# Kernel optimization log

Measured on AMD Instinct MI355X. Metric: run time of the kernel, lower is better.

The kernel has to match this reference:

```python
import jax, jax.numpy as jnp
import numpy as np

N, E, G = 8192, 65536, 16          # atoms, edges, graphs in batch
NUM_ELEM, C, NB = 10, 64, 8        # elements, hidden channels, bessel basis
LMAX, NLAYERS = 3, 2
LM = (LMAX + 1) ** 2               # 16 spherical-harmonic components
R_MAX, P_CUT = 5.0, 5
EPS = 1e-9


def spherical_harmonics(u):
    # u: [E,3] unit vectors -> real spherical harmonics l<=3, [E,16]
    x, y, z = u[:, 0], u[:, 1], u[:, 2]
    x2, y2, z2 = x * x, y * y, z * z
    sh = [
        jnp.full_like(x, 0.28209479177387814),
        0.4886025119029199 * y, 0.4886025119029199 * z, 0.4886025119029199 * x,
        1.0925484305920792 * x * y, 1.0925484305920792 * y * z,
        0.31539156525252005 * (3.0 * z2 - 1.0),
        1.0925484305920792 * x * z, 0.5462742152960396 * (x2 - y2),
        0.5900435899266435 * y * (3.0 * x2 - y2), 2.890611442640554 * x * y * z,
        0.4570457994644658 * y * (5.0 * z2 - 1.0),
        0.3731763325901154 * z * (5.0 * z2 - 3.0),
        0.4570457994644658 * x * (5.0 * z2 - 1.0),
        1.445305721320277 * z * (x2 - y2),
        0.5900435899266435 * x * (x2 - 3.0 * y2),
    ]
    return jnp.stack(sh, axis=-1)


def radial_embedding(r):
    # Bessel radial basis with polynomial envelope cutoff -> [E, NB]
    u = r / R_MAX
    p = float(P_CUT)
    cut = (1.0 - 0.5 * (p + 1.0) * (p + 2.0) * u ** P_CUT
           + p * (p + 2.0) * u ** (P_CUT + 1)
           - 0.5 * p * (p + 1.0) * u ** (P_CUT + 2))
    cut = jnp.where(u < 1.0, cut, 0.0)
    n = jnp.arange(1, NB + 1, dtype=r.dtype)
    bessel = jnp.sqrt(2.0 / R_MAX) * jnp.sin(n[None, :] * jnp.pi * u[:, None]) \
             / jnp.maximum(r, EPS)[:, None]
    return bessel * cut[:, None]


def setup_inputs() -> dict:
    key = jax.random.key(0)
    ks = jax.random.split(key, 10)
    positions = jax.random.uniform(ks[0], (N, 3), jnp.float32) * 10.0
    elems = jax.random.randint(ks[1], (N,), 0, NUM_ELEM)
    node_attrs = jax.nn.one_hot(elems, NUM_ELEM, dtype=jnp.float32)
    edge_index = jax.random.randint(ks[2], (2, E), 0, N).astype(jnp.int32)
    shifts = jnp.zeros((E, 3), jnp.float32)
    batch = jnp.sort(jax.random.randint(ks[3], (N,), 0, G)).astype(jnp.int32)
    W_embed = jax.random.normal(ks[4], (NUM_ELEM, C), jnp.float32) / np.sqrt(NUM_ELEM)
    atomic_energies_w = jnp.arange(-1.0, -(NUM_ELEM + 1.0), -1.0, dtype=jnp.float32)
    W_rad = jax.random.normal(ks[5], (NLAYERS, NB, C), jnp.float32) / np.sqrt(NB)
    W_prod = jax.random.normal(ks[6], (NLAYERS, NUM_ELEM, (LMAX + 1) * C, C),
                               jnp.float32) / np.sqrt((LMAX + 1) * C)
    w_read = jax.random.normal(ks[7], (C,), jnp.float32) / np.sqrt(C)
    return {"positions": positions, "node_attrs": node_attrs, "shifts": shifts,
            "W_embed": W_embed, "atomic_energies_w": atomic_energies_w,
            "W_rad": W_rad, "W_prod": W_prod, "w_read": w_read,
            "edge_index": edge_index, "batch": batch}


def _energy(positions, node_attrs, shifts, W_embed, atomic_energies_w,
            W_rad, W_prod, w_read, edge_index, batch):
    snd, rcv = edge_index[0], edge_index[1]
    vec = positions[rcv] - positions[snd] + shifts            # [E,3]
    length = jnp.sqrt(jnp.sum(vec * vec, axis=-1) + EPS)      # [E]
    Y = spherical_harmonics(vec / length[:, None])            # [E,LM]
    R = radial_embedding(length)                              # [E,NB]

    e0 = jax.ops.segment_sum(node_attrs @ atomic_energies_w, batch, num_segments=G)
    h = node_attrs @ W_embed                                  # [N,C]

    for layer in range(NLAYERS):
        w = R @ W_rad[layer]                                  # [E,C] radial weights
        msg = (w * h[snd])[:, None, :] * Y[:, :, None]        # [E,LM,C] tensor product
        A = jax.ops.segment_sum(msg, rcv, num_segments=N)     # [N,LM,C] atomic basis
        A2 = A * A
        # invariant (rotation-invariant) contraction: sum over m within each l
        B = jnp.concatenate(
            [A2[:, l * l:(l + 1) * (l + 1), :].sum(axis=1) for l in range(LMAX + 1)],
            axis=-1)                                          # [N,(LMAX+1)*C]
        # element-dependent product-basis mixing
        h = jnp.einsum('nf,efc,ne->nc', B, W_prod[layer], node_attrs)

    node_e = h @ w_read                                       # [N]
    inter_e = jax.ops.segment_sum(node_e, batch, num_segments=G)
    return e0 + inter_e                                       # [G]


def reference(positions, node_attrs, shifts, W_embed, atomic_energies_w,
              W_rad, W_prod, w_read, edge_index, batch):
    energy = _energy(positions, node_attrs, shifts, W_embed, atomic_energies_w,
                     W_rad, W_prod, w_read, edge_index, batch)
    forces = -jax.grad(
        lambda p: _energy(p, node_attrs, shifts, W_embed, atomic_energies_w,
                          W_rad, W_prod, w_read, edge_index, batch).sum()
    )(positions)
    return energy, forces
```

## Files before the change

kernel.cpp:

```cpp
#include <hip/hip_runtime.h>
#include <math.h>

#define NN 8192
#define NE 65536
#define NG 16
#define NEL 10
#define CC 64
#define NLM 16
#define MAXST 32
#define PI_F 3.14159265358979f

__device__ __forceinline__ int lm_l(int lm) {
    return (lm == 0) ? 0 : (lm < 4) ? 1 : (lm < 9) ? 2 : 3;
}

__device__ __forceinline__ void stage_pack(
    const float* __restrict__ PK, const int* __restrict__ SSND,
    int beg, int cnt, int c, float* sPK, int* sS)
{
    int tot = cnt * 24;
    for (int i = c; i < tot; i += 64) sPK[i] = PK[(size_t)beg*24 + i];
    if (c < cnt) sS[c] = SSND[beg + c];
    __builtin_amdgcn_wave_barrier();
}

__global__ __launch_bounds__(256) void k_front(
    const float* __restrict__ pos, const float* __restrict__ shifts,
    const int* __restrict__ snd, const int* __restrict__ rcv,
    float* __restrict__ Y, float* __restrict__ R,
    float* __restrict__ U, float* __restrict__ L, int* __restrict__ cnt,
    const float* __restrict__ attrs, const float* __restrict__ Wemb,
    const float* __restrict__ aew, const int* __restrict__ batch,
    float* __restrict__ h0, int* __restrict__ elem, int* __restrict__ ecnt,
    float* __restrict__ out,
    const float* __restrict__ Wprod1, const float* __restrict__ wread,
    float* __restrict__ vb1)
{
    __shared__ int hcnt[NEL];
    int bx = blockIdx.x;
    if (bx < 256) {
        int e = bx * 256 + threadIdx.x;
        int s = snd[e], r = rcv[e];
        float vx = pos[r*3+0] - pos[s*3+0] + shifts[e*3+0];
        float vy = pos[r*3+1] - pos[s*3+1] + shifts[e*3+1];
        float vz = pos[r*3+2] - pos[s*3+2] + shifts[e*3+2];
        float len = sqrtf(vx*vx + vy*vy + vz*vz + 1e-9f);
        L[e] = len;
        if (len >= 5.0f) return;
        atomicAdd(&cnt[r], 1);
        float x = vx/len, y = vy/len, z = vz/len;
        U[e*3+0] = x; U[e*3+1] = y; U[e*3+2] = z;
        float x2 = x*x, y2 = y*y, z2 = z*z;
        float4* Yv = (float4*)(Y + (size_t)e*16);
        Yv[0] = make_float4(0.28209479177387814f,
                            0.4886025119029199f*y,
                            0.4886025119029199f*z,
                            0.4886025119029199f*x);
        Yv[1] = make_float4(1.0925484305920792f*x*y,
                            1.0925484305920792f*y*z,
                            0.31539156525252005f*(3.f*z2 - 1.f),
                            1.0925484305920792f*x*z);
        Yv[2] = make_float4(0.5462742152960396f*(x2 - y2),
                            0.5900435899266435f*y*(3.f*x2 - y2),
                            2.890611442640554f*x*y*z,
                            0.4570457994644658f*y*(5.f*z2 - 1.f));
        Yv[3] = make_float4(0.3731763325901154f*z*(5.f*z2 - 3.f),
                            0.4570457994644658f*x*(5.f*z2 - 1.f),
                            1.445305721320277f*z*(x2 - y2),
                            0.5900435899266435f*x*(x2 - 3.f*y2));
        float ur = len * 0.2f;
        float u2 = ur*ur, u4 = u2*u2, u5 = u4*ur, u6 = u5*ur, u7 = u6*ur;
        float cut = 1.f - 21.f*u5 + 35.f*u6 - 15.f*u7;
        const float s2f = 0.632455532033676f;
        float th = (PI_F/5.f) * len;
        float s1, c1; sincosf(th, &s1, &c1);
        float sn_ = s1, cs = c1;
        float coef = s2f * cut / len;
        float rv[8];
#pragma unroll
        for (int nb = 0; nb < 8; nb++) {
            rv[nb] = coef * sn_;
            float ns = sn_*c1 + cs*s1;
            float nc = cs*c1 - sn_*s1;
            sn_ = ns; cs = nc;
        }
        float4* Rv = (float4*)(R + (size_t)e*8);
        Rv[0] = make_float4(rv[0], rv[1], rv[2], rv[3]);
        Rv[1] = make_float4(rv[4], rv[5], rv[6], rv[7]);
    } else if (bx < 768) {
        int t = threadIdx.x, c = t & 63, w = t >> 6;
        if (t < NEL) hcnt[t] = 0;
        __syncthreads();
        float esum = 0.f; int curb = -1;
        for (int g = 0; g < 4; g++) {
            int n = (bx - 256)*16 + w*4 + g;
            float hv = 0.f;
            for (int el = 0; el < NEL; el++) hv += attrs[n*NEL+el] * Wemb[el*CC+c];
            h0[(size_t)n*CC+c] = hv;
            int el = 0; float e0 = 0.f;
            for (int k = 0; k < NEL; k++) {
                float a = attrs[n*NEL+k];
                e0 += a * aew[k];
                if (a > 0.5f) el = k;
            }
            if (c == 0) {
                elem[n] = el;
                atomicAdd(&hcnt[el], 1);
            }
            int b = batch[n];
            if (b != curb) {
                if (curb >= 0 && c == 0) atomicAdd(&out[curb], esum);
                curb = b; esum = 0.f;
            }
            esum += e0;
        }
        if (curb >= 0 && c == 0) atomicAdd(&out[curb], esum);
        __syncthreads();
        if (t < NEL) { int v = hcnt[t]; if (v) atomicAdd(&ecnt[t], v); }
    } else {
        int el = bx - 768, f = threadIdx.x;
        float s = 0.f;
        for (int c = 0; c < CC; c++) s += wread[c] * Wprod1[(size_t)el*256*CC + f*CC + c];
        vb1[el*256+f] = s;
    }
}

__global__ __launch_bounds__(1024) void k_scan(
    const int* __restrict__ cnt, int* __restrict__ offs,
    const int* __restrict__ ecnt, int* __restrict__ eoff)
{
    __shared__ int wsum[16];
    int t = threadIdx.x, lane = t & 63, w = t >> 6;
    int loc[8];
    int run = 0;
#pragma unroll
    for (int i = 0; i < 8; i++) { int v = cnt[t*8+i]; loc[i] = run; run += v; }
    int v = run;
#pragma unroll
    for (int o = 1; o < 64; o <<= 1) {
        int u = __shfl_up(v, o, 64);
        if (lane >= o) v += u;
    }
    if (lane == 63) wsum[w] = v;
    __syncthreads();
    if (t < 16) {
        int x = wsum[t];
#pragma unroll
        for (int o = 1; o < 16; o <<= 1) {
            int u = __shfl_up(x, o, 64);
            if (t >= o) x += u;
        }
        wsum[t] = x;
    }
    __syncthreads();
    int wpre = (w == 0) ? 0 : wsum[w-1];
    int pre = wpre + v - run;
#pragma unroll
    for (int i = 0; i < 8; i++) offs[t*8+i] = pre + loc[i];
    if (t == 1023) offs[NN] = pre + run;
    if (t == 0) {
        int r = 0;
        for (int el = 0; el < NEL; el++) { eoff[el] = r; r += ecnt[el]; }
        eoff[NEL] = r;
    }
}

__global__ void k_scatpack(
    const int* __restrict__ snd, const int* __restrict__ rcv,
    const float* __restrict__ Y, const float* __restrict__ R,
    const float* __restrict__ U, const float* __restrict__ L,
    const int* __restrict__ offs, int* __restrict__ cur,
    float* __restrict__ PK, int* __restrict__ SSND, int* __restrict__ SRCV,
    float* __restrict__ UL,
    const int* __restrict__ elem, const int* __restrict__ eoff,
    int* __restrict__ ecur, int* __restrict__ nbe)
{
    int e = blockIdx.x * blockDim.x + threadIdx.x;
    if (e < NN) {
        int el = elem[e];
        int p = eoff[el] + atomicAdd(&ecur[el], 1);
        nbe[p] = e;
    }
    if (e >= NE) return;
    if (L[e] >= 5.0f) return;
    int r = rcv[e];
    int p = offs[r] + atomicAdd(&cur[r], 1);
    const float4* Yp = (const float4*)(Y + (size_t)e*16);
    float4* d = (float4*)(PK + (size_t)p*24);
    d[0] = Yp[0]; d[1] = Yp[1]; d[2] = Yp[2]; d[3] = Yp[3];
    const float4* Rp = (const float4*)(R + (size_t)e*8);
    d[4] = Rp[0]; d[5] = Rp[1];
    SSND[p] = snd[e];
    SRCV[p] = rcv[e];
    ((float4*)UL)[p] = make_float4(U[e*3+0], U[e*3+1], U[e*3+2], L[e]);
}

__global__ __launch_bounds__(256) void k_fwd0(
    const float* __restrict__ PK, const int* __restrict__ SSND,
    const float* __restrict__ Wrad0, const float* __restrict__ Wprod0,
    const float* __restrict__ h0, const float* __restrict__ attrs,
    const int* __restrict__ elem, const int* __restrict__ offs,
    const int* __restrict__ nbe, float* __restrict__ h1,
    float* __restrict__ A0)
{
    __shared__ __align__(16) float sB[4][1024];
    __shared__ __align__(16) float sPK[4][MAXST*24];
    __shared__ int sS[4][MAXST];
    int t = threadIdx.x, c = t & 63, w = t >> 6;
    float wr[8];
#pragma unroll
    for (int nb = 0; nb < 8; nb++) wr[nb] = Wrad0[nb*CC+c];
    int nid[4], nel[4]; float na[4];
#pragma unroll
    for (int g = 0; g < 4; g++) {
        int n = nbe[blockIdx.x*16 + w*4 + g];
        nid[g] = n;
        int el = elem[n]; nel[g] = el; na[g] = attrs[n*NEL+el];
        float acc[NLM];
#pragma unroll
        for (int lm = 0; lm < NLM; lm++) acc[lm] = 0.f;
        int beg = offs[n], end = offs[n+1];
        for (int base = beg; base < end; base += MAXST) {
            int m = min(MAXST, end - base);
            stage_pack(PK, SSND, base, m, c, sPK[w], sS[w]);
            for (int cb = 0; cb < m; cb += 4) {
                float hb[4];
#pragma unroll
                for (int k = 0; k < 4; k++)
                    hb[k] = (cb+k < m) ? h0[(size_t)sS[w][cb+k]*CC + c] : 0.f;
#pragma unroll
                for (int jj = 0; jj < 4; jj++) {
                    if (cb+jj >= m) break;
                    const float* rec = &sPK[w][(cb+jj)*24];
                    float wv = 0.f;
#pragma unroll
                    for (int nb = 0; nb < 8; nb++) wv += rec[16+nb]*wr[nb];
                    float tt = wv * hb[jj];
#pragma unroll
                    for (int lm = 0; lm < NLM; lm++) acc[lm] += rec[lm]*tt;
                }
            }
            __builtin_amdgcn_wave_barrier();
        }
#pragma unroll
        for (int lm = 0; lm < NLM; lm++) A0[(size_t)n*1024 + lm*64 + c] = acc[lm];
        float b0 = acc[0]*acc[0];
        float b1 = acc[1]*acc[1] + acc[2]*acc[2] + acc[3]*acc[3];
        float b2 = acc[4]*acc[4] + acc[5]*acc[5] + acc[6]*acc[6] + acc[7]*acc[7] + acc[8]*acc[8];
        float b3 = 0.f;
#pragma unroll
        for (int lm = 9; lm < 16; lm++) b3 += acc[lm]*acc[lm];
        sB[w][g*256 + 0*64 + c] = b0;
        sB[w][g*256 + 1*64 + c] = b1;
        sB[w][g*256 + 2*64 + c] = b2;
        sB[w][g*256 + 3*64 + c] = b3;
    }
    __builtin_amdgcn_wave_barrier();
    float hv[4] = {0.f, 0.f, 0.f, 0.f};
    int done = 0;
    while (done != 0xF) {
        int g0 = __ffs(~done & 0xF) - 1;
        int el = (g0==0) ? nel[0] : (g0==1) ? nel[1] : (g0==2) ? nel[2] : nel[3];
        int msk = 0;
#pragma unroll
        for (int g = 0; g < 4; g++) if (nel[g] == el) msk |= 1 << g;
        const float* Wn = Wprod0 + (size_t)el*256*CC;
        float tmp[4] = {0.f, 0.f, 0.f, 0.f};
        for (int f4 = 0; f4 < 64; f4++) {
            float wv0 = Wn[(f4*4+0)*CC + c];
            float wv1 = Wn[(f4*4+1)*CC + c];
            float wv2 = Wn[(f4*4+2)*CC + c];
            float wv3 = Wn[(f4*4+3)*CC + c];
#pragma unroll
            for (int g = 0; g < 4; g++) {
                float4 b = *((const float4*)&sB[w][g*256 + f4*4]);
                tmp[g] += b.x*wv0 + b.y*wv1 + b.z*wv2 + b.w*wv3;
            }
        }
#pragma unroll
        for (int g = 0; g < 4; g++) if ((msk >> g) & 1) hv[g] = tmp[g];
        done |= msk;
    }
#pragma unroll
    for (int g = 0; g < 4; g++) h1[(size_t)nid[g]*CC + c] = na[g]*hv[g];
}

__global__ __launch_bounds__(256) void k_gseed(
    const float* __restrict__ gh1, const float* __restrict__ Wprod0,
    const float* __restrict__ attrs, const int* __restrict__ elem,
    const int* __restrict__ nbe, float* __restrict__ GB)
{
    __shared__ __align__(16) float sgh[4][4][64];
    int t = threadIdx.x, c = t & 63, w = t >> 6;
    int nid[4], nel[4]; float na[4];
#pragma unroll
    for (int g = 0; g < 4; g++) {
        int n = nbe[blockIdx.x*16 + w*4 + g];
        nid[g] = n;
        int el = elem[n]; nel[g] = el; na[g] = attrs[n*NEL+el];
        sgh[w][g][c] = gh1[(size_t)n*CC + c];
    }
    __builtin_amdgcn_wave_barrier();
    float outv[4][4];
    int done = 0;
    while (done != 0xF) {
        int g0 = __ffs(~done & 0xF) - 1;
        int el = (g0==0) ? nel[0] : (g0==1) ? nel[1] : (g0==2) ? nel[2] : nel[3];
        int msk = 0;
#pragma unroll
        for (int g = 0; g < 4; g++) if (nel[g] == el) msk |= 1 << g;
        const float* W0 = Wprod0 + (size_t)el*256*CC;
#pragma unroll
        for (int l = 0; l < 4; l++) {
            const float4* row = (const float4*)(W0 + (size_t)(l*64 + c)*CC);
            float t4[4] = {0.f, 0.f, 0.f, 0.f};
#pragma unroll 4
            for (int k4 = 0; k4 < 16; k4++) {
                float4 wv = row[k4];
#pragma unroll
                for (int g = 0; g < 4; g++) {
                    float4 gg = *((const float4*)&sgh[w][g][k4*4]);
                    t4[g] += wv.x*gg.x + wv.y*gg.y + wv.z*gg.z + wv.w*gg.w;
                }
            }
#pragma unroll
            for (int g = 0; g < 4; g++) if ((msk >> g) & 1) outv[l][g] = t4[g];
        }
        done |= msk;
    }
#pragma unroll
    for (int g = 0; g < 4; g++)
#pragma unroll
        for (int l = 0; l < 4; l++)
            GB[(size_t)nid[g]*256 + l*64 + c] = na[g]*outv[l][g];
}

__global__ __launch_bounds__(256) void k_fbwd(
    const float* __restrict__ PK, const int* __restrict__ SSND,
    const float* __restrict__ Wrad, const float* __restrict__ hprev,
    const float* __restrict__ vb1, const float* __restrict__ GB,
    const float* __restrict__ A0,
    const float* __restrict__ attrs, const int* __restrict__ elem,
    const int* __restrict__ batch, const int* __restrict__ offs,
    float* __restrict__ gYp, float* __restrict__ gRp, float* __restrict__ gh,
    float* __restrict__ out, int layer1)
{
    __shared__ __align__(16) float wrls[8*68];
    __shared__ __align__(16) float sPK[4][MAXST*24];
    __shared__ int sS[4][MAXST];
    __shared__ __align__(16) float Mls[4][16*68];
    __shared__ __align__(16) float Tls[4][4*68];
    __shared__ __align__(16) float Gls[4][4*68];
    int t = threadIdx.x, c = t & 63, w = t >> 6;
    float wr[8];
#pragma unroll
    for (int nb = 0; nb < 8; nb++) wr[nb] = Wrad[nb*CC+c];
    if (w == 0) {
#pragma unroll
        for (int nb = 0; nb < 8; nb++) wrls[nb*68+c] = wr[nb];
    }
    __syncthreads();
    float esum = 0.f; int curb = -1;
    for (int g = 0; g < 4; g++) {
        int n = blockIdx.x*16 + w*4 + g;
        int el = elem[n];
        float a = attrs[n*NEL+el];
        float g4[4];
        if (layer1) {
#pragma unroll
            for (int l = 0; l < 4; l++) g4[l] = a * vb1[el*256 + l*64 + c];
        } else {
#pragma unroll
            for (int l = 0; l < 4; l++) g4[l] = GB[(size_t)n*256 + l*64 + c];
        }
        int beg = offs[n], end = offs[n+1];
        int cnt = end - beg;
        float acc[NLM];
        bool cached = false;
        if (layer1) {
#pragma unroll
            for (int lm = 0; lm < NLM; lm++) acc[lm] = 0.f;
            for (int base = beg; base < end; base += MAXST) {
                int m = min(MAXST, end - base);
                stage_pack(PK, SSND, base, m, c, sPK[w], sS[w]);
                for (int cb = 0; cb < m; cb += 4) {
                    float hb[4];
#pragma unroll
                    for (int k = 0; k < 4; k++)
                        hb[k] = (cb+k < m) ? hprev[(size_t)sS[w][cb+k]*CC + c] : 0.f;
#pragma unroll
                    for (int jj = 0; jj < 4; jj++) {
                        if (cb+jj >= m) break;
                        const float* rec = &sPK[w][(cb+jj)*24];
                        float wv = 0.f;
#pragma unroll
                        for (int nb = 0; nb < 8; nb++) wv += rec[16+nb]*wr[nb];
                        float tt = wv * hb[jj];
#pragma unroll
                        for (int lm = 0; lm < NLM; lm++) acc[lm] += rec[lm]*tt;
                    }
                }
                __builtin_amdgcn_wave_barrier();
            }
            cached = (cnt <= MAXST);
            float b0 = acc[0]*acc[0];
            float b1 = acc[1]*acc[1] + acc[2]*acc[2] + acc[3]*acc[3];
            float b2 = acc[4]*acc[4] + acc[5]*acc[5] + acc[6]*acc[6] + acc[7]*acc[7] + acc[8]*acc[8];
            float b3 = 0.f;
#pragma unroll
            for (int lm = 9; lm < 16; lm++) b3 += acc[lm]*acc[lm];
            float ep = b0*vb1[el*256+c] + b1*vb1[el*256+64+c]
                     + b2*vb1[el*256+128+c] + b3*vb1[el*256+192+c];
#pragma unroll
            for (int o = 32; o > 0; o >>= 1) ep += __shfl_xor(ep, o, 64);
            int b = batch[n];
            if (b != curb) {
                if (curb >= 0 && c == 0) atomicAdd(&out[curb], esum);
                curb = b; esum = 0.f;
            }
            esum += a * ep;
        } else {
#pragma unroll
            for (int lm = 0; lm < NLM; lm++) acc[lm] = A0[(size_t)n*1024 + lm*64 + c];
        }
        float M[NLM];
#pragma unroll
        for (int lm = 0; lm < NLM; lm++) {
            M[lm] = 2.f * acc[lm] * g4[lm_l(lm)];
            Mls[w][lm*68+c] = M[lm];
        }
        __builtin_amdgcn_wave_barrier();
        for (int base = beg; base < end; base += MAXST) {
            int m = min(MAXST, end - base);
            if (!cached) stage_pack(PK, SSND, base, m, c, sPK[w], sS[w]);
            for (int cb = 0; cb < m; cb += 4) {
                int ncq = min(4, m - cb);
                float hb[4];
#pragma unroll
                for (int k = 0; k < 4; k++)
                    hb[k] = (cb+k < m) ? hprev[(size_t)sS[w][cb+k]*CC + c] : 0.f;
#pragma unroll
                for (int jj = 0; jj < 4; jj++) {
                    if (jj >= ncq) break;
                    const float* rec = &sPK[w][(cb+jj)*24];
                    float wv = 0.f;
#pragma unroll
                    for (int nb = 0; nb < 8; nb++) wv += rec[16+nb]*wr[nb];
                    float hvv = hb[jj];
                    float my = 0.f;
#pragma unroll
                    for (int lm = 0; lm < NLM; lm++) my += M[lm]*rec[lm];
                    Tls[w][jj*68+c] = wv * hvv;
                    Gls[w][jj*68+c] = hvv * my;
                    if (layer1) atomicAdd(&gh[(size_t)sS[w][cb+jj]*CC + c], wv * my);
                }
                __builtin_amdgcn_wave_barrier();
                {
                    int jj = c >> 4, lm = c & 15;
                    if (jj < ncq) {
                        const float4* mrow = (const float4*)&Mls[w][lm*68];
                        const float4* trow = (const float4*)&Tls[w][jj*68];
                        float s_ = 0.f;
#pragma unroll
                        for (int k4 = 0; k4 < 16; k4++) {
                            float4 mm = mrow[k4]; float4 tv = trow[k4];
                            s_ += mm.x*tv.x + mm.y*tv.y + mm.z*tv.z + mm.w*tv.w;
                        }
                        size_t p = (size_t)(base + cb + jj);
                        if (layer1) gYp[p*16+lm] = s_;
                        else        gYp[p*16+lm] += s_;
                    }
                }
                if (c < 32) {
                    int jj = c >> 3, nb = c & 7;
                    if (jj < ncq) {
                        const float4* wrow = (const float4*)&wrls[nb*68];
                        const float4* grow = (const float4*)&Gls[w][jj*68];
                        float s_ = 0.f;
#pragma unroll
                        for (int k4 = 0; k4 < 16; k4++) {
                            float4 wv4 = wrow[k4]; float4 gv = grow[k4];
                            s_ += wv4.x*gv.x + wv4.y*gv.y + wv4.z*gv.z + wv4.w*gv.w;
                        }
                        size_t p = (size_t)(base + cb + jj);
                        if (layer1) gRp[p*8+nb] = s_;
                        else        gRp[p*8+nb] += s_;
                    }
                }
                __builtin_amdgcn_wave_barrier();
            }
        }
    }
    if (curb >= 0 && c == 0) atomicAdd(&out[curb], esum);
}

__global__ void k_geo_bwd(const float* __restrict__ gYp, const float* __restrict__ gRp,
                          const float* __restrict__ UL, const int* __restrict__ SSND,
                          const int* __restrict__ SRCV, const int* __restrict__ offs,
                          float* __restrict__ F)
{
    int p = blockIdx.x * blockDim.x + threadIdx.x;
    if (p >= offs[NN]) return;
    float4 ul = ((const float4*)UL)[p];
    float x = ul.x, y = ul.y, z = ul.z, len = ul.w;
    float g[16];
    {
        const float4* gv = (const float4*)(gYp + (size_t)p*16);
        float4 a0 = gv[0], a1 = gv[1], a2 = gv[2], a3 = gv[3];
        g[0]=a0.x; g[1]=a0.y; g[2]=a0.z; g[3]=a0.w;
        g[4]=a1.x; g[5]=a1.y; g[6]=a1.z; g[7]=a1.w;
        g[8]=a2.x; g[9]=a2.y; g[10]=a2.z; g[11]=a2.w;
        g[12]=a3.x; g[13]=a3.y; g[14]=a3.z; g[15]=a3.w;
    }
    float gr[8];
    {
        const float4* rv = (const float4*)(gRp + (size_t)p*8);
        float4 r0 = rv[0], r1 = rv[1];
        gr[0]=r0.x; gr[1]=r0.y; gr[2]=r0.z; gr[3]=r0.w;
        gr[4]=r1.x; gr[5]=r1.y; gr[6]=r1.z; gr[7]=r1.w;
    }
    float x2 = x*x, y2 = y*y, z2 = z*z;
    float gx = 0.f, gy = 0.f, gz = 0.f;
    gx += 0.4886025119029199f*g[3];
    gy += 0.4886025119029199f*g[1];
    gz += 0.4886025119029199f*g[2];
    gx += 1.0925484305920792f*y*g[4];  gy += 1.0925484305920792f*x*g[4];
    gy += 1.0925484305920792f*z*g[5];  gz += 1.0925484305920792f*y*g[5];
    gz += 1.8923493915151203f*z*g[6];
    gx += 1.0925484305920792f*z*g[7];  gz += 1.0925484305920792f*x*g[7];
    gx += 1.0925484305920792f*x*g[8];  gy -= 1.0925484305920792f*y*g[8];
    gx += 3.540261539559861f*x*y*g[9];
    gy += 0.5900435899266435f*(3.f*x2 - 3.f*y2)*g[9];
    gx += 2.890611442640554f*y*z*g[10]; gy += 2.890611442640554f*x*z*g[10]; gz += 2.890611442640554f*x*y*g[10];
    gy += 0.4570457994644658f*(5.f*z2 - 1.f)*g[11]; gz += 4.570457994644658f*y*z*g[11];
    gz += 0.3731763325901154f*(15.f*z2 - 3.f)*g[12];
    gx += 0.4570457994644658f*(5.f*z2 - 1.f)*g[13]; gz += 4.570457994644658f*x*z*g[13];
    gx += 2.890611442640554f*x*z*g[14]; gy -= 2.890611442640554f*y*z*g[14];
    gz += 1.445305721320277f*(x2 - y2)*g[14];
    gx += 0.5900435899266435f*(3.f*x2 - 3.f*y2)*g[15];
    gy -= 3.540261539559861f*x*y*g[15];
    float ur = len * 0.2f;
    float gL = 0.f;
    {
        float u2 = ur*ur, u4 = u2*u2, u5 = u4*ur, u6 = u5*ur, u7 = u6*ur;
        float poly  = 1.f - 21.f*u5 + 35.f*u6 - 15.f*u7;
        float dpoly = (-105.f*u4 + 210.f*u5 - 105.f*u6)*0.2f;
        const float s2f = 0.632455532033676f;
        const float k1 = PI_F/5.f;
        float th = k1*len;
        float s1, c1; sincosf(th, &s1, &c1);
        float sn_ = s1, cs = c1;
        float inv_r = 1.f/len;
        bool tiny = (len < 2e-3f);
#pragma unroll
        for (int nb = 0; nb < 8; nb++) {
            float kn = k1*(float)(nb+1);
            float bes = s2f*sn_*inv_r;
            float dbes;
            if (tiny) dbes = -s2f*kn*kn*kn*len*(1.f/3.f);
            else      dbes = s2f*(kn*cs - sn_*inv_r)*inv_r;
            gL += gr[nb]*(dbes*poly + bes*dpoly);
            float ns = sn_*c1 + cs*s1;
            float nc = cs*c1 - sn_*s1;
            sn_ = ns; cs = nc;
        }
    }
    float dot = gx*x + gy*y + gz*z;
    float gvx = (gx - dot*x)/len + gL*x;
    float gvy = (gy - dot*y)/len + gL*y;
    float gvz = (gz - dot*z)/len + gL*z;
    int sn = SSND[p], rn = SRCV[p];
    atomicAdd(&F[rn*3+0], -gvx);
    atomicAdd(&F[rn*3+1], -gvy);
    atomicAdd(&F[rn*3+2], -gvz);
    atomicAdd(&F[sn*3+0],  gvx);
    atomicAdd(&F[sn*3+1],  gvy);
    atomicAdd(&F[sn*3+2],  gvz);
}

extern "C" void kernel_launch(void* const* d_in, const int* in_sizes, int n_in,
                              void* d_out, int out_size, void* d_ws, size_t ws_size,
                              hipStream_t stream)
{
    const float* positions  = (const float*)d_in[0];
    const float* node_attrs = (const float*)d_in[1];
    const float* shifts     = (const float*)d_in[2];
    const float* W_embed    = (const float*)d_in[3];
    const float* aew        = (const float*)d_in[4];
    const float* W_rad      = (const float*)d_in[5];
    const float* W_prod     = (const float*)d_in[6];
    const float* w_read     = (const float*)d_in[7];
    const int*   edge_index = (const int*)d_in[8];
    const int*   batch      = (const int*)d_in[9];
    float* out = (float*)d_out;

    const int* snd = edge_index;
    const int* rcv = edge_index + NE;

    char* ws = (char*)d_ws;
    size_t off = 0;
    auto allocf = [&](size_t nelems) -> float* {
        float* p = (float*)(ws + off); off += nelems * sizeof(float); return p;
    };
    float* Y    = allocf((size_t)NE*16);
    float* R    = allocf((size_t)NE*8);
    float* U    = allocf((size_t)NE*3);
    float* L    = allocf((size_t)NE);
    float* PK   = allocf((size_t)NE*24);
    float* UL   = allocf((size_t)NE*4);
    float* H0   = allocf((size_t)NN*CC);
    float* H1   = allocf((size_t)NN*CC);
    float* A0   = allocf((size_t)NN*1024);
    float* GYP  = allocf((size_t)NE*16);
    float* GRP  = allocf((size_t)NE*8);
    float* GB   = allocf((size_t)NN*256);
    float* VB1  = allocf((size_t)NEL*256);
    size_t zero_off = off;
    float* GH1  = allocf((size_t)NN*CC);
    int* CNT   = (int*)(ws + off); off += (size_t)NN*4;
    int* CUR   = (int*)(ws + off); off += (size_t)NN*4;
    int* ECNT  = (int*)(ws + off); off += 16*4;
    int* ECUR  = (int*)(ws + off); off += 16*4;
    size_t zero_bytes = off - zero_off;
    int* ELEM  = (int*)(ws + off); off += (size_t)NN*4;
    int* OFFS  = (int*)(ws + off); off += (size_t)(NN+1)*4;
    int* SSND  = (int*)(ws + off); off += (size_t)NE*4;
    int* SRCV  = (int*)(ws + off); off += (size_t)NE*4;
    int* ELOFF = (int*)(ws + off); off += 16*4;
    int* NBE   = (int*)(ws + off); off += (size_t)NN*4;

    hipMemsetAsync(out, 0, (size_t)out_size * sizeof(float), stream);
    hipMemsetAsync(ws + zero_off, 0, zero_bytes, stream);

    const float* Wrad0  = W_rad;
    const float* Wrad1  = W_rad + 8*CC;
    const float* Wprod0 = W_prod;
    const float* Wprod1 = W_prod + (size_t)NEL*256*CC;

    k_front<<<256 + 512 + NEL, 256, 0, stream>>>(
        positions, shifts, snd, rcv, Y, R, U, L, CNT,
        node_attrs, W_embed, aew, batch, H0, ELEM, ECNT, out,
        Wprod1, w_read, VB1);
    k_scan<<<1, 1024, 0, stream>>>(CNT, OFFS, ECNT, ELOFF);
    k_scatpack<<<NE/256, 256, 0, stream>>>(snd, rcv, Y, R, U, L, OFFS, CUR,
                                           PK, SSND, SRCV, UL, ELEM, ELOFF, ECUR, NBE);

    k_fwd0<<<NN/16, 256, 0, stream>>>(PK, SSND, Wrad0, Wprod0, H0, node_attrs, ELEM,
                                      OFFS, NBE, H1, A0);
    k_fbwd<<<NN/16, 256, 0, stream>>>(PK, SSND, Wrad1, H1, VB1, GB, A0, node_attrs, ELEM,
                                      batch, OFFS, GYP, GRP, GH1, out, 1);
    k_gseed<<<NN/16, 256, 0, stream>>>(GH1, Wprod0, node_attrs, ELEM, NBE, GB);
    k_fbwd<<<NN/16, 256, 0, stream>>>(PK, SSND, Wrad0, H0, VB1, GB, A0, node_attrs, ELEM,
                                      batch, OFFS, GYP, GRP, GH1, out, 0);

    k_geo_bwd<<<NE/256, 256, 0, stream>>>(GYP, GRP, UL, SSND, SRCV, OFFS, out + NG);
    (void)in_sizes; (void)n_in; (void)ws_size;
}
```

Before: 288.1 us.

## Fuse gradient seed, layer-0 backward and geometric force backward into one kernel

Splits the shared backward kernel into a layer-1 specialization and a new layer-0 kernel. The new kernel computes the product-basis gradient seed in registers, adds it to the layer-1 edge gradients, and computes per-edge force contributions inline. This removes the GB buffer, the SRCV array, the read-modify-write of gYp/gRp, and two kernel launches. In exchange, the serial per-edge geometry math now runs on only 4 lanes per wave inside the edge loop, which may cut lane utilisation. Layer-0 node order now follows the element-sorted list, which changes the atomic patterns.

```diff
diff --git a/kernel.cpp b/kernel.cpp
--- a/kernel.cpp
+++ b/kernel.cpp
@@ -170,7 +170,7 @@
     const float* __restrict__ Y, const float* __restrict__ R,
     const float* __restrict__ U, const float* __restrict__ L,
     const int* __restrict__ offs, int* __restrict__ cur,
-    float* __restrict__ PK, int* __restrict__ SSND, int* __restrict__ SRCV,
+    float* __restrict__ PK, int* __restrict__ SSND,
     float* __restrict__ UL,
     const int* __restrict__ elem, const int* __restrict__ eoff,
     int* __restrict__ ecur, int* __restrict__ nbe)
@@ -191,7 +191,6 @@
     const float4* Rp = (const float4*)(R + (size_t)e*8);
     d[4] = Rp[0]; d[5] = Rp[1];
     SSND[p] = snd[e];
-    SRCV[p] = rcv[e];
     ((float4*)UL)[p] = make_float4(U[e*3+0], U[e*3+1], U[e*3+2], L[e]);
 }
 
@@ -285,65 +284,14 @@
     for (int g = 0; g < 4; g++) h1[(size_t)nid[g]*CC + c] = na[g]*hv[g];
 }
 
-__global__ __launch_bounds__(256) void k_gseed(
-    const float* __restrict__ gh1, const float* __restrict__ Wprod0,
-    const float* __restrict__ attrs, const int* __restrict__ elem,
-    const int* __restrict__ nbe, float* __restrict__ GB)
-{
-    __shared__ __align__(16) float sgh[4][4][64];
-    int t = threadIdx.x, c = t & 63, w = t >> 6;
-    int nid[4], nel[4]; float na[4];
-#pragma unroll
-    for (int g = 0; g < 4; g++) {
-        int n = nbe[blockIdx.x*16 + w*4 + g];
-        nid[g] = n;
-        int el = elem[n]; nel[g] = el; na[g] = attrs[n*NEL+el];
-        sgh[w][g][c] = gh1[(size_t)n*CC + c];
-    }
-    __builtin_amdgcn_wave_barrier();
-    float outv[4][4];
-    int done = 0;
-    while (done != 0xF) {
-        int g0 = __ffs(~done & 0xF) - 1;
-        int el = (g0==0) ? nel[0] : (g0==1) ? nel[1] : (g0==2) ? nel[2] : nel[3];
-        int msk = 0;
-#pragma unroll
-        for (int g = 0; g < 4; g++) if (nel[g] == el) msk |= 1 << g;
-        const float* W0 = Wprod0 + (size_t)el*256*CC;
-#pragma unroll
-        for (int l = 0; l < 4; l++) {
-            const float4* row = (const float4*)(W0 + (size_t)(l*64 + c)*CC);
-            float t4[4] = {0.f, 0.f, 0.f, 0.f};
-#pragma unroll 4
-            for (int k4 = 0; k4 < 16; k4++) {
-                float4 wv = row[k4];
-#pragma unroll
-                for (int g = 0; g < 4; g++) {
-                    float4 gg = *((const float4*)&sgh[w][g][k4*4]);
-                    t4[g] += wv.x*gg.x + wv.y*gg.y + wv.z*gg.z + wv.w*gg.w;
-                }
-            }
-#pragma unroll
-            for (int g = 0; g < 4; g++) if ((msk >> g) & 1) outv[l][g] = t4[g];
-        }
-        done |= msk;
-    }
-#pragma unroll
-    for (int g = 0; g < 4; g++)
-#pragma unroll
-        for (int l = 0; l < 4; l++)
-            GB[(size_t)nid[g]*256 + l*64 + c] = na[g]*outv[l][g];
-}
-
-__global__ __launch_bounds__(256) void k_fbwd(
+__global__ __launch_bounds__(256) void k_fbwd1(
     const float* __restrict__ PK, const int* __restrict__ SSND,
-    const float* __restrict__ Wrad, const float* __restrict__ hprev,
-    const float* __restrict__ vb1, const float* __restrict__ GB,
-    const float* __restrict__ A0,
+    const float* __restrict__ Wrad1, const float* __restrict__ h1,
+    const float* __restrict__ vb1,
     const float* __restrict__ attrs, const int* __restrict__ elem,
     const int* __restrict__ batch, const int* __restrict__ offs,
     float* __restrict__ gYp, float* __restrict__ gRp, float* __restrict__ gh,
-    float* __restrict__ out, int layer1)
+    float* __restrict__ out)
 {
     __shared__ __align__(16) float wrls[8*68];
     __shared__ __align__(16) float sPK[4][MAXST*24];
@@ -354,7 +302,7 @@
     int t = threadIdx.x, c = t & 63, w = t >> 6;
     float wr[8];
 #pragma unroll
-    for (int nb = 0; nb < 8; nb++) wr[nb] = Wrad[nb*CC+c];
+    for (int nb = 0; nb < 8; nb++) wr[nb] = Wrad1[nb*CC+c];
     if (w == 0) {
 #pragma unroll
         for (int nb = 0; nb < 8; nb++) wrls[nb*68+c] = wr[nb];
@@ -366,63 +314,52 @@
         int el = elem[n];
         float a = attrs[n*NEL+el];
         float g4[4];
-        if (layer1) {
-#pragma unroll
-            for (int l = 0; l < 4; l++) g4[l] = a * vb1[el*256 + l*64 + c];
-        } else {
-#pragma unroll
-            for (int l = 0; l < 4; l++) g4[l] = GB[(size_t)n*256 + l*64 + c];
-        }
+#pragma unroll
+        for (int l = 0; l < 4; l++) g4[l] = a * vb1[el*256 + l*64 + c];
         int beg = offs[n], end = offs[n+1];
         int cnt = end - beg;
         float acc[NLM];
-        bool cached = false;
-        if (layer1) {
-#pragma unroll
-            for (int lm = 0; lm < NLM; lm++) acc[lm] = 0.f;
-            for (int base = beg; base < end; base += MAXST) {
-                int m = min(MAXST, end - base);
-                stage_pack(PK, SSND, base, m, c, sPK[w], sS[w]);
-                for (int cb = 0; cb < m; cb += 4) {
-                    float hb[4];
-#pragma unroll
-                    for (int k = 0; k < 4; k++)
-                        hb[k] = (cb+k < m) ? hprev[(size_t)sS[w][cb+k]*CC + c] : 0.f;
-#pragma unroll
-                    for (int jj = 0; jj < 4; jj++) {
-                        if (cb+jj >= m) break;
-                        const float* rec = &sPK[w][(cb+jj)*24];
-                        float wv = 0.f;
-#pragma unroll
-                        for (int nb = 0; nb < 8; nb++) wv += rec[16+nb]*wr[nb];
-                        float tt = wv * hb[jj];
-#pragma unroll
-                        for (int lm = 0; lm < NLM; lm++) acc[lm] += rec[lm]*tt;
-                    }
-                }
-                __builtin_amdgcn_wave_barrier();
-            }
-            cached = (cnt <= MAXST);
-            float b0 = acc[0]*acc[0];
-            float b1 = acc[1]*acc[1] + acc[2]*acc[2] + acc[3]*acc[3];
-            float b2 = acc[4]*acc[4] + acc[5]*acc[5] + acc[6]*acc[6] + acc[7]*acc[7] + acc[8]*acc[8];
-            float b3 = 0.f;
-#pragma unroll
-            for (int lm = 9; lm < 16; lm++) b3 += acc[lm]*acc[lm];
-            float ep = b0*vb1[el*256+c] + b1*vb1[el*256+64+c]
-                     + b2*vb1[el*256+128+c] + b3*vb1[el*256+192+c];
-#pragma unroll
-            for (int o = 32; o > 0; o >>= 1) ep += __shfl_xor(ep, o, 64);
-            int b = batch[n];
-            if (b != curb) {
-                if (curb >= 0 && c == 0) atomicAdd(&out[curb], esum);
-                curb = b; esum = 0.f;
-            }
-            esum += a * ep;
-        } else {
-#pragma unroll
-            for (int lm = 0; lm < NLM; lm++) acc[lm] = A0[(size_t)n*1024 + lm*64 + c];
-        }
+#pragma unroll
+        for (int lm = 0; lm < NLM; lm++) acc[lm] = 0.f;
+        for (int base = beg; base < end; base += MAXST) {
+            int m = min(MAXST, end - base);
+            stage_pack(PK, SSND, base, m, c, sPK[w], sS[w]);
+            for (int cb = 0; cb < m; cb += 4) {
+                float hb[4];
+#pragma unroll
+                for (int k = 0; k < 4; k++)
+                    hb[k] = (cb+k < m) ? h1[(size_t)sS[w][cb+k]*CC + c] : 0.f;
+#pragma unroll
+                for (int jj = 0; jj < 4; jj++) {
+                    if (cb+jj >= m) break;
+                    const float* rec = &sPK[w][(cb+jj)*24];
+                    float wv = 0.f;
+#pragma unroll
+                    for (int nb = 0; nb < 8; nb++) wv += rec[16+nb]*wr[nb];
+                    float tt = wv * hb[jj];
+#pragma unroll
+                    for (int lm = 0; lm < NLM; lm++) acc[lm] += rec[lm]*tt;
+                }
+            }
+            __builtin_amdgcn_wave_barrier();
+        }
+        bool cached = (cnt <= MAXST);
+        float b0 = acc[0]*acc[0];
+        float b1 = acc[1]*acc[1] + acc[2]*acc[2] + acc[3]*acc[3];
+        float b2 = acc[4]*acc[4] + acc[5]*acc[5] + acc[6]*acc[6] + acc[7]*acc[7] + acc[8]*acc[8];
+        float b3 = 0.f;
+#pragma unroll
+        for (int lm = 9; lm < 16; lm++) b3 += acc[lm]*acc[lm];
+        float ep = b0*vb1[el*256+c] + b1*vb1[el*256+64+c]
+                 + b2*vb1[el*256+128+c] + b3*vb1[el*256+192+c];
+#pragma unroll
+        for (int o = 32; o > 0; o >>= 1) ep += __shfl_xor(ep, o, 64);
+        int b = batch[n];
+        if (b != curb) {
+            if (curb >= 0 && c == 0) atomicAdd(&out[curb], esum);
+            curb = b; esum = 0.f;
+        }
+        esum += a * ep;
         float M[NLM];
 #pragma unroll
         for (int lm = 0; lm < NLM; lm++) {
@@ -438,7 +375,7 @@
                 float hb[4];
 #pragma unroll
                 for (int k = 0; k < 4; k++)
-                    hb[k] = (cb+k < m) ? hprev[(size_t)sS[w][cb+k]*CC + c] : 0.f;
+                    hb[k] = (cb+k < m) ? h1[(size_t)sS[w][cb+k]*CC + c] : 0.f;
 #pragma unroll
                 for (int jj = 0; jj < 4; jj++) {
                     if (jj >= ncq) break;
@@ -452,7 +389,7 @@
                     for (int lm = 0; lm < NLM; lm++) my += M[lm]*rec[lm];
                     Tls[w][jj*68+c] = wv * hvv;
                     Gls[w][jj*68+c] = hvv * my;
-                    if (layer1) atomicAdd(&gh[(size_t)sS[w][cb+jj]*CC + c], wv * my);
+                    atomicAdd(&gh[(size_t)sS[w][cb+jj]*CC + c], wv * my);
                 }
                 __builtin_amdgcn_wave_barrier();
                 {
@@ -466,9 +403,7 @@
                             float4 mm = mrow[k4]; float4 tv = trow[k4];
                             s_ += mm.x*tv.x + mm.y*tv.y + mm.z*tv.z + mm.w*tv.w;
                         }
-                        size_t p = (size_t)(base + cb + jj);
-                        if (layer1) gYp[p*16+lm] = s_;
-                        else        gYp[p*16+lm] += s_;
+                        gYp[(size_t)(base + cb + jj)*16+lm] = s_;
                     }
                 }
                 if (c < 32) {
@@ -482,9 +417,7 @@
                             float4 wv4 = wrow[k4]; float4 gv = grow[k4];
                             s_ += wv4.x*gv.x + wv4.y*gv.y + wv4.z*gv.z + wv4.w*gv.w;
                         }
-                        size_t p = (size_t)(base + cb + jj);
-                        if (layer1) gRp[p*8+nb] = s_;
-                        else        gRp[p*8+nb] += s_;
+                        gRp[(size_t)(base + cb + jj)*8+nb] = s_;
                     }
                 }
                 __builtin_amdgcn_wave_barrier();
@@ -494,88 +427,206 @@
     if (curb >= 0 && c == 0) atomicAdd(&out[curb], esum);
 }
 
-__global__ void k_geo_bwd(const float* __restrict__ gYp, const float* __restrict__ gRp,
-                          const float* __restrict__ UL, const int* __restrict__ SSND,
-                          const int* __restrict__ SRCV, const int* __restrict__ offs,
-                          float* __restrict__ F)
+__global__ __launch_bounds__(256) void k_fbwd0geo(
+    const float* __restrict__ PK, const int* __restrict__ SSND,
+    const float* __restrict__ Wrad0, const float* __restrict__ h0,
+    const float* __restrict__ gh1, const float* __restrict__ Wprod0,
+    const float* __restrict__ A0,
+    const float* __restrict__ attrs, const int* __restrict__ elem,
+    const int* __restrict__ offs, const int* __restrict__ nbe,
+    const float* __restrict__ gYp, const float* __restrict__ gRp,
+    const float* __restrict__ UL, float* __restrict__ F)
 {
-    int p = blockIdx.x * blockDim.x + threadIdx.x;
-    if (p >= offs[NN]) return;
-    float4 ul = ((const float4*)UL)[p];
-    float x = ul.x, y = ul.y, z = ul.z, len = ul.w;
-    float g[16];
-    {
-        const float4* gv = (const float4*)(gYp + (size_t)p*16);
-        float4 a0 = gv[0], a1 = gv[1], a2 = gv[2], a3 = gv[3];
-        g[0]=a0.x; g[1]=a0.y; g[2]=a0.z; g[3]=a0.w;
-        g[4]=a1.x; g[5]=a1.y; g[6]=a1.z; g[7]=a1.w;
-        g[8]=a2.x; g[9]=a2.y; g[10]=a2.z; g[11]=a2.w;
-        g[12]=a3.x; g[13]=a3.y; g[14]=a3.z; g[15]=a3.w;
-    }
-    float gr[8];
-    {
-        const float4* rv = (const float4*)(gRp + (size_t)p*8);
-        float4 r0 = rv[0], r1 = rv[1];
-        gr[0]=r0.x; gr[1]=r0.y; gr[2]=r0.z; gr[3]=r0.w;
-        gr[4]=r1.x; gr[5]=r1.y; gr[6]=r1.z; gr[7]=r1.w;
-    }
-    float x2 = x*x, y2 = y*y, z2 = z*z;
-    float gx = 0.f, gy = 0.f, gz = 0.f;
-    gx += 0.4886025119029199f*g[3];
-    gy += 0.4886025119029199f*g[1];
-    gz += 0.4886025119029199f*g[2];
-    gx += 1.0925484305920792f*y*g[4];  gy += 1.0925484305920792f*x*g[4];
-    gy += 1.0925484305920792f*z*g[5];  gz += 1.0925484305920792f*y*g[5];
-    gz += 1.8923493915151203f*z*g[6];
-    gx += 1.0925484305920792f*z*g[7];  gz += 1.0925484305920792f*x*g[7];
-    gx += 1.0925484305920792f*x*g[8];  gy -= 1.0925484305920792f*y*g[8];
-    gx += 3.540261539559861f*x*y*g[9];
-    gy += 0.5900435899266435f*(3.f*x2 - 3.f*y2)*g[9];
-    gx += 2.890611442640554f*y*z*g[10]; gy += 2.890611442640554f*x*z*g[10]; gz += 2.890611442640554f*x*y*g[10];
-    gy += 0.4570457994644658f*(5.f*z2 - 1.f)*g[11]; gz += 4.570457994644658f*y*z*g[11];
-    gz += 0.3731763325901154f*(15.f*z2 - 3.f)*g[12];
-    gx += 0.4570457994644658f*(5.f*z2 - 1.f)*g[13]; gz += 4.570457994644658f*x*z*g[13];
-    gx += 2.890611442640554f*x*z*g[14]; gy -= 2.890611442640554f*y*z*g[14];
-    gz += 1.445305721320277f*(x2 - y2)*g[14];
-    gx += 0.5900435899266435f*(3.f*x2 - 3.f*y2)*g[15];
-    gy -= 3.540261539559861f*x*y*g[15];
-    float ur = len * 0.2f;
-    float gL = 0.f;
-    {
-        float u2 = ur*ur, u4 = u2*u2, u5 = u4*ur, u6 = u5*ur, u7 = u6*ur;
-        float poly  = 1.f - 21.f*u5 + 35.f*u6 - 15.f*u7;
-        float dpoly = (-105.f*u4 + 210.f*u5 - 105.f*u6)*0.2f;
-        const float s2f = 0.632455532033676f;
-        const float k1 = PI_F/5.f;
-        float th = k1*len;
-        float s1, c1; sincosf(th, &s1, &c1);
-        float sn_ = s1, cs = c1;
-        float inv_r = 1.f/len;
-        bool tiny = (len < 2e-3f);
-#pragma unroll
-        for (int nb = 0; nb < 8; nb++) {
-            float kn = k1*(float)(nb+1);
-            float bes = s2f*sn_*inv_r;
-            float dbes;
-            if (tiny) dbes = -s2f*kn*kn*kn*len*(1.f/3.f);
-            else      dbes = s2f*(kn*cs - sn_*inv_r)*inv_r;
-            gL += gr[nb]*(dbes*poly + bes*dpoly);
-            float ns = sn_*c1 + cs*s1;
-            float nc = cs*c1 - sn_*s1;
-            sn_ = ns; cs = nc;
-        }
-    }
-    float dot = gx*x + gy*y + gz*z;
-    float gvx = (gx - dot*x)/len + gL*x;
-    float gvy = (gy - dot*y)/len + gL*y;
-    float gvz = (gz - dot*z)/len + gL*z;
-    int sn = SSND[p], rn = SRCV[p];
-    atomicAdd(&F[rn*3+0], -gvx);
-    atomicAdd(&F[rn*3+1], -gvy);
-    atomicAdd(&F[rn*3+2], -gvz);
-    atomicAdd(&F[sn*3+0],  gvx);
-    atomicAdd(&F[sn*3+1],  gvy);
-    atomicAdd(&F[sn*3+2],  gvz);
+    __shared__ __align__(16) float wrls[8*68];
+    __shared__ __align__(16) float sPK[4][MAXST*24];
+    __shared__ int sS[4][MAXST];
+    __shared__ __align__(16) float Mls[4][16*68];
+    __shared__ __align__(16) float Tls[4][4*68];
+    __shared__ __align__(16) float Gls[4][4*68];
+    __shared__ __align__(16) float sgh[4][4][64];
+    __shared__ float gols[4][4*24];
+    int t = threadIdx.x, c = t & 63, w = t >> 6;
+    float wr[8];
+#pragma unroll
+    for (int nb = 0; nb < 8; nb++) wr[nb] = Wrad0[nb*CC+c];
+    if (w == 0) {
+#pragma unroll
+        for (int nb = 0; nb < 8; nb++) wrls[nb*68+c] = wr[nb];
+    }
+    __syncthreads();
+    int nid[4], nel[4]; float na[4];
+#pragma unroll
+    for (int g = 0; g < 4; g++) {
+        int n = nbe[blockIdx.x*16 + w*4 + g];
+        nid[g] = n;
+        int el = elem[n]; nel[g] = el; na[g] = attrs[n*NEL+el];
+        sgh[w][g][c] = gh1[(size_t)n*CC + c];
+    }
+    __builtin_amdgcn_wave_barrier();
+    float outv[4][4];
+    int done = 0;
+    while (done != 0xF) {
+        int g0 = __ffs(~done & 0xF) - 1;
+        int el = (g0==0) ? nel[0] : (g0==1) ? nel[1] : (g0==2) ? nel[2] : nel[3];
+        int msk = 0;
+#pragma unroll
+        for (int g = 0; g < 4; g++) if (nel[g] == el) msk |= 1 << g;
+        const float* W0 = Wprod0 + (size_t)el*256*CC;
+#pragma unroll
+        for (int l = 0; l < 4; l++) {
+            const float4* row = (const float4*)(W0 + (size_t)(l*64 + c)*CC);
+            float t4[4] = {0.f, 0.f, 0.f, 0.f};
+#pragma unroll 4
+            for (int k4 = 0; k4 < 16; k4++) {
+                float4 wv = row[k4];
+#pragma unroll
+                for (int g = 0; g < 4; g++) {
+                    float4 gg = *((const float4*)&sgh[w][g][k4*4]);
+                    t4[g] += wv.x*gg.x + wv.y*gg.y + wv.z*gg.z + wv.w*gg.w;
+                }
+            }
+#pragma unroll
+            for (int g = 0; g < 4; g++) if ((msk >> g) & 1) outv[l][g] = t4[g];
+        }
+        done |= msk;
+    }
+    for (int g = 0; g < 4; g++) {
+        int n = nid[g];
+        float g4[4];
+#pragma unroll
+        for (int l = 0; l < 4; l++) g4[l] = na[g]*outv[l][g];
+        int beg = offs[n], end = offs[n+1];
+        float acc[NLM];
+#pragma unroll
+        for (int lm = 0; lm < NLM; lm++) acc[lm] = A0[(size_t)n*1024 + lm*64 + c];
+        float M[NLM];
+#pragma unroll
+        for (int lm = 0; lm < NLM; lm++) {
+            M[lm] = 2.f * acc[lm] * g4[lm_l(lm)];
+            Mls[w][lm*68+c] = M[lm];
+        }
+        __builtin_amdgcn_wave_barrier();
+        for (int base = beg; base < end; base += MAXST) {
+            int m = min(MAXST, end - base);
+            stage_pack(PK, SSND, base, m, c, sPK[w], sS[w]);
+            for (int cb = 0; cb < m; cb += 4) {
+                int ncq = min(4, m - cb);
+                float hb[4];
+#pragma unroll
+                for (int k = 0; k < 4; k++)
+                    hb[k] = (cb+k < m) ? h0[(size_t)sS[w][cb+k]*CC + c] : 0.f;
+#pragma unroll
+                for (int jj = 0; jj < 4; jj++) {
+                    if (jj >= ncq) break;
+                    const float* rec = &sPK[w][(cb+jj)*24];
+                    float wv = 0.f;
+#pragma unroll
+                    for (int nb = 0; nb < 8; nb++) wv += rec[16+nb]*wr[nb];
+                    float hvv = hb[jj];
+                    float my = 0.f;
+#pragma unroll
+                    for (int lm = 0; lm < NLM; lm++) my += M[lm]*rec[lm];
+                    Tls[w][jj*68+c] = wv * hvv;
+                    Gls[w][jj*68+c] = hvv * my;
+                }
+                __builtin_amdgcn_wave_barrier();
+                {
+                    int jj = c >> 4, lm = c & 15;
+                    if (jj < ncq) {
+                        const float4* mrow = (const float4*)&Mls[w][lm*68];
+                        const float4* trow = (const float4*)&Tls[w][jj*68];
+                        float s_ = 0.f;
+#pragma unroll
+                        for (int k4 = 0; k4 < 16; k4++) {
+                            float4 mm = mrow[k4]; float4 tv = trow[k4];
+                            s_ += mm.x*tv.x + mm.y*tv.y + mm.z*tv.z + mm.w*tv.w;
+                        }
+                        gols[w][jj*24+lm] = s_ + gYp[(size_t)(base + cb + jj)*16+lm];
+                    }
+                }
+                if (c < 32) {
+                    int jj = c >> 3, nb = c & 7;
+                    if (jj < ncq) {
+                        const float4* wrow = (const float4*)&wrls[nb*68];
+                        const float4* grow = (const float4*)&Gls[w][jj*68];
+                        float s_ = 0.f;
+#pragma unroll
+                        for (int k4 = 0; k4 < 16; k4++) {
+                            float4 wv4 = wrow[k4]; float4 gv = grow[k4];
+                            s_ += wv4.x*gv.x + wv4.y*gv.y + wv4.z*gv.z + wv4.w*gv.w;
+                        }
+                        gols[w][jj*24+16+nb] = s_ + gRp[(size_t)(base + cb + jj)*8+nb];
+                    }
+                }
+                __builtin_amdgcn_wave_barrier();
+                if ((c & 15) == 0) {
+                    int jj = c >> 4;
+                    if (jj < ncq) {
+                        int p = base + cb + jj;
+                        const float* go = &gols[w][jj*24];
+                        float4 ul = ((const float4*)UL)[p];
+                        float x = ul.x, y = ul.y, z = ul.z, len = ul.w;
+                        float x2 = x*x, y2 = y*y, z2 = z*z;
+                        float gx = 0.f, gy = 0.f, gz = 0.f;
+                        gx += 0.4886025119029199f*go[3];
+                        gy += 0.4886025119029199f*go[1];
+                        gz += 0.4886025119029199f*go[2];
+                        gx += 1.0925484305920792f*y*go[4];  gy += 1.0925484305920792f*x*go[4];
+                        gy += 1.0925484305920792f*z*go[5];  gz += 1.0925484305920792f*y*go[5];
+                        gz += 1.8923493915151203f*z*go[6];
+                        gx += 1.0925484305920792f*z*go[7];  gz += 1.0925484305920792f*x*go[7];
+                        gx += 1.0925484305920792f*x*go[8];  gy -= 1.0925484305920792f*y*go[8];
+                        gx += 3.540261539559861f*x*y*go[9];
+                        gy += 0.5900435899266435f*(3.f*x2 - 3.f*y2)*go[9];
+                        gx += 2.890611442640554f*y*z*go[10]; gy += 2.890611442640554f*x*z*go[10]; gz += 2.890611442640554f*x*y*go[10];
+                        gy += 0.4570457994644658f*(5.f*z2 - 1.f)*go[11]; gz += 4.570457994644658f*y*z*go[11];
+                        gz += 0.3731763325901154f*(15.f*z2 - 3.f)*go[12];
+                        gx += 0.4570457994644658f*(5.f*z2 - 1.f)*go[13]; gz += 4.570457994644658f*x*z*go[13];
+                        gx += 2.890611442640554f*x*z*go[14]; gy -= 2.890611442640554f*y*z*go[14];
+                        gz += 1.445305721320277f*(x2 - y2)*go[14];
+                        gx += 0.5900435899266435f*(3.f*x2 - 3.f*y2)*go[15];
+                        gy -= 3.540261539559861f*x*y*go[15];
+                        float ur = len * 0.2f;
+                        float u2 = ur*ur, u4 = u2*u2, u5 = u4*ur, u6 = u5*ur, u7 = u6*ur;
+                        float poly  = 1.f - 21.f*u5 + 35.f*u6 - 15.f*u7;
+                        float dpoly = (-105.f*u4 + 210.f*u5 - 105.f*u6)*0.2f;
+                        const float s2f = 0.632455532033676f;
+                        const float k1 = PI_F/5.f;
+                        float th = k1*len;
+                        float s1, c1; sincosf(th, &s1, &c1);
+                        float sn_ = s1, cs = c1;
+                        float inv_r = 1.f/len;
+                        bool tiny = (len < 2e-3f);
+                        float gL = 0.f;
+#pragma unroll
+                        for (int nb = 0; nb < 8; nb++) {
+                            float kn = k1*(float)(nb+1);
+                            float bes = s2f*sn_*inv_r;
+                            float dbes;
+                            if (tiny) dbes = -s2f*kn*kn*kn*len*(1.f/3.f);
+                            else      dbes = s2f*(kn*cs - sn_*inv_r)*inv_r;
+                            gL += go[16+nb]*(dbes*poly + bes*dpoly);
+                            float ns = sn_*c1 + cs*s1;
+                            float nc = cs*c1 - sn_*s1;
+                            sn_ = ns; cs = nc;
+                        }
+                        float dot = gx*x + gy*y + gz*z;
+                        float gvx = (gx - dot*x)*inv_r + gL*x;
+                        float gvy = (gy - dot*y)*inv_r + gL*y;
+                        float gvz = (gz - dot*z)*inv_r + gL*z;
+                        int sn2 = sS[w][cb+jj];
+                        atomicAdd(&F[n*3+0], -gvx);
+                        atomicAdd(&F[n*3+1], -gvy);
+                        atomicAdd(&F[n*3+2], -gvz);
+                        atomicAdd(&F[sn2*3+0],  gvx);
+                        atomicAdd(&F[sn2*3+1],  gvy);
+                        atomicAdd(&F[sn2*3+2],  gvz);
+                    }
+                }
+                __builtin_amdgcn_wave_barrier();
+            }
+        }
+    }
 }
 
 extern "C" void kernel_launch(void* const* d_in, const int* in_sizes, int n_in,
@@ -613,7 +664,6 @@
     float* A0   = allocf((size_t)NN*1024);
     float* GYP  = allocf((size_t)NE*16);
     float* GRP  = allocf((size_t)NE*8);
-    float* GB   = allocf((size_t)NN*256);
     float* VB1  = allocf((size_t)NEL*256);
     size_t zero_off = off;
     float* GH1  = allocf((size_t)NN*CC);
@@ -625,7 +675,6 @@
     int* ELEM  = (int*)(ws + off); off += (size_t)NN*4;
     int* OFFS  = (int*)(ws + off); off += (size_t)(NN+1)*4;
     int* SSND  = (int*)(ws + off); off += (size_t)NE*4;
-    int* SRCV  = (int*)(ws + off); off += (size_t)NE*4;
     int* ELOFF = (int*)(ws + off); off += 16*4;
     int* NBE   = (int*)(ws + off); off += (size_t)NN*4;
 
@@ -643,16 +692,14 @@
         Wprod1, w_read, VB1);
     k_scan<<<1, 1024, 0, stream>>>(CNT, OFFS, ECNT, ELOFF);
     k_scatpack<<<NE/256, 256, 0, stream>>>(snd, rcv, Y, R, U, L, OFFS, CUR,
-                                           PK, SSND, SRCV, UL, ELEM, ELOFF, ECUR, NBE);
+                                           PK, SSND, UL, ELEM, ELOFF, ECUR, NBE);
 
     k_fwd0<<<NN/16, 256, 0, stream>>>(PK, SSND, Wrad0, Wprod0, H0, node_attrs, ELEM,
                                       OFFS, NBE, H1, A0);
-    k_fbwd<<<NN/16, 256, 0, stream>>>(PK, SSND, Wrad1, H1, VB1, GB, A0, node_attrs, ELEM,
-                                      batch, OFFS, GYP, GRP, GH1, out, 1);
-    k_gseed<<<NN/16, 256, 0, stream>>>(GH1, Wprod0, node_attrs, ELEM, NBE, GB);
-    k_fbwd<<<NN/16, 256, 0, stream>>>(PK, SSND, Wrad0, H0, VB1, GB, A0, node_attrs, ELEM,
-                                      batch, OFFS, GYP, GRP, GH1, out, 0);
-
-    k_geo_bwd<<<NE/256, 256, 0, stream>>>(GYP, GRP, UL, SSND, SRCV, OFFS, out + NG);
+    k_fbwd1<<<NN/16, 256, 0, stream>>>(PK, SSND, Wrad1, H1, VB1, node_attrs, ELEM,
+                                       batch, OFFS, GYP, GRP, GH1, out);
+    k_fbwd0geo<<<NN/16, 256, 0, stream>>>(PK, SSND, Wrad0, H0, GH1, Wprod0, A0,
+                                          node_attrs, ELEM, OFFS, NBE,
+                                          GYP, GRP, UL, out + NG);
     (void)in_sizes; (void)n_in; (void)ws_size;
 }
```

Result: faster. 275.1 us (-4.5%).
